# Kernel optimization log

Measured on AMD Instinct MI355X. Metric: run time of the kernel, lower is better.

The kernel has to match this reference:

```python
import jax, jax.numpy as jnp
import numpy as np

B, NCAP, LV, LT, C = 64, 64, 197, 32, 512
NSP = LV - 1          # 196 spatial patches
NUM_KEEP = 98         # ceil(196 * sparse_ratio=0.5)
KEEPED = 49           # int(196 * aggr_ratio=0.5 * sparse_ratio=0.5)
HID = 102             # int(512 * dim_ratio=0.2)
LN_EPS = 1e-5


def _normalize(x):
    # torch F.normalize: x / max(||x||, 1e-12)
    return x / jnp.maximum(jnp.linalg.norm(x, axis=-1, keepdims=True), 1e-12)


def setup_inputs() -> dict:
    key = jax.random.key(0)
    ks = jax.random.split(key, 8)
    def rn(k, shape, s=0.02):
        return jax.random.normal(k, shape, jnp.float32) * s
    return {
        "img_embs": jax.random.normal(ks[0], (B, LV, C), jnp.float32),
        "cap_embs": jax.random.normal(ks[1], (NCAP, LT, C), jnp.float32),
        "cap_lens": jnp.full((NCAP,), LT, jnp.int32),
        "ln_gamma": jnp.ones((C,), jnp.float32),
        "ln_beta": jnp.zeros((C,), jnp.float32),
        "w1": rn(ks[2], (C, HID)), "b1": jnp.zeros((HID,), jnp.float32),
        "w2": rn(ks[3], (HID, KEEPED)), "b2": jnp.zeros((KEEPED,), jnp.float32),
        "aggr_scale": jnp.ones((1, 1, 1), jnp.float32),
        "wi2t": rn(ks[4], (C, C)), "bi2t": jnp.zeros((C,), jnp.float32),
        "wt2i": rn(ks[5], (C, C)), "bt2i": jnp.zeros((C,), jnp.float32),
        "temp": jnp.ones((1, 1, 1), jnp.float32),
    }


def _forward(img_embs, cap_embs, ln_gamma, ln_beta, w1, b1, w2, b2,
             aggr_scale, wi2t, bi2t, wt2i, bt2i, temp):
    img_norm = _normalize(img_embs)
    img_cls = img_embs[:, 0:1]              # [B,1,C]  has_cls_token branch
    img_sp = img_embs[:, 1:]                # [B,196,C]
    img_sp_norm = img_norm[:, 1:]
    # use_cls_as_glob_embd: global = normalized CLS (no grad)
    glo = jax.lax.stop_gradient(img_norm[:, 0:1])
    attn_x = jax.lax.stop_gradient(jnp.sum(glo * img_sp_norm, -1))  # [B,196]
    cap_norm = _normalize(cap_embs)
    bidx = jnp.arange(B)[:, None]

    def ln(x):
        m = x.mean(-1, keepdims=True)
        v = jnp.var(x, axis=-1, keepdims=True)
        return (x - m) / jnp.sqrt(v + LN_EPS) * ln_gamma + ln_beta

    def per_caption(cap_i, cap_i_norm):
        # cap_i, cap_i_norm: [LT, C]
        cap_glo = jax.lax.stop_gradient(_normalize(cap_i[0:1]))           # [1,C]
        attn_y = jax.lax.stop_gradient(jnp.sum(cap_glo[None] * img_sp_norm, -1))  # [B,196]
        # --- TokenSparse ---
        score = attn_x + attn_y
        order = jnp.argsort(-score, axis=1)                              # descending
        keep, nonkeep = order[:, :NUM_KEEP], order[:, NUM_KEEP:]
        sel = img_sp[bidx, keep]                                          # [B,98,C]
        non = img_sp[bidx, nonkeep]                                       # [B,98,C]
        non_score = jnp.take_along_axis(score, nonkeep, 1)
        extra = jnp.sum(non * jax.nn.softmax(non_score, axis=1)[..., None],
                        axis=1, keepdims=True)                            # [B,1,C]
        # --- TokenAggregation ---
        h = jax.nn.gelu(ln(sel) @ w1 + b1, approximate=False)             # [B,98,HID]
        w = jnp.swapaxes(h @ w2 + b2, 1, 2) * aggr_scale                  # [B,49,98]
        aggr = jax.nn.softmax(w, axis=2) @ sel                            # [B,49,C]
        # [cls, aggr, extra] -> [B,51,C], then normalize
        sel_tok = _normalize(jnp.concatenate([img_cls, aggr, extra], 1))
        Ls = sel_tok.shape[1]
        # --- 'attn' similarity ---
        cap_exp = jnp.broadcast_to(cap_i_norm[None], (B, LT, C))
        st = jnp.swapaxes(sel_tok, 1, 2)                                  # [B,C,51]
        c2i = jax.nn.leaky_relu(cap_exp @ st, negative_slope=0.1)         # [B,LT,51]
        a_i2t = jax.nn.softmax((cap_exp @ wi2t + bi2t) @ st / temp, axis=1)
        a_t2i = jax.nn.softmax((cap_exp @ wt2i + bt2i) @ st / temp, axis=2)
        return jnp.sum(a_i2t * c2i / Ls + a_t2i * c2i / LT, axis=(1, 2))  # [B]

    sims = jax.vmap(per_caption)(cap_embs, cap_norm)                      # [NCAP,B]
    return sims.T                                                         # [B,NCAP]


def reference(img_embs, cap_embs, cap_lens, ln_gamma, ln_beta, w1, b1, w2, b2,
              aggr_scale, wi2t, bi2t, wt2i, bt2i, temp):
    # cap_lens are all LT (static shapes); eval-mode output: similarity matrix.
    return _forward(img_embs, cap_embs, ln_gamma, ln_beta, w1, b1, w2, b2,
                    aggr_scale, wi2t, bi2t, wt2i, bt2i, temp)
```

## Files before the change

kernel.cpp:

```cpp
#include <hip/hip_runtime.h>
#include <math.h>

#define B     64
#define NCAP  64
#define LV    197
#define LT    32
#define C     512
#define NSP   196
#define NKEEP 98
#define HID   102
#define KEEPED 49

#define OFF_ATTNX   12608
#define OFF_WSMAT   25152
#define OFF_WT      639808
#define OFF_GLOT    1688384
#define OFF_ATTNYT  1721152
#define OFF_IMGT    14164800
#define OFF_QBB     17834816
#define OFF_QCAP    19407680
#define OFF_W1TF    19931968
#define OFF_W2TF    19960640

typedef unsigned int u32;
typedef unsigned short u16;
typedef __bf16 bf16x8 __attribute__((ext_vector_type(8)));
typedef float f32x4 __attribute__((ext_vector_type(4)));
typedef unsigned int uint4v __attribute__((ext_vector_type(4)));

__device__ __forceinline__ u16 f2bf(float f) {
    u32 u = __builtin_bit_cast(u32, f);
    return (u16)((u + 0x7FFFu + ((u >> 16) & 1u)) >> 16);
}
__device__ __forceinline__ bf16x8 ld_bf8(const u16* p) {
    uint4v v = *reinterpret_cast<const uint4v*>(p);
    return __builtin_bit_cast(bf16x8, v);
}

__device__ __forceinline__ float gelu_exact(float x) {
    return 0.5f * x * (1.f + erff(x * 0.70710678118654752f));
}

__global__ __launch_bounds__(256) void k_pre(const float* __restrict__ img,
                                             const float* __restrict__ cap,
                                             const float* __restrict__ wi2t,
                                             const float* __restrict__ wt2i,
                                             const float* __restrict__ w1,
                                             const float* __restrict__ w2,
                                             u16* __restrict__ imgTf,
                                             float* __restrict__ gloT,
                                             u16* __restrict__ Qbbf,
                                             u16* __restrict__ Qcap,
                                             u16* __restrict__ wT,
                                             u16* __restrict__ w1Tf,
                                             u16* __restrict__ w2Tf) {
    int idx = blockIdx.x, t = threadIdx.x;
    __shared__ __align__(16) u16 shb[64 * 224];

    if (idx < 512) {
        int b = idx >> 3, cg = idx & 7;
        for (int f = t; f < 64 * 27; f += 256) shb[(f / 27) * 224 + 197 + (f % 27)] = 0;
        int cc = t & 63;
        for (int sb = t >> 6; sb < 197; sb += 4) {
            float v = img[((size_t)b * LV + sb) * C + cg * 64 + cc];
            shb[cc * 224 + sb] = f2bf(v);
        }
        __syncthreads();
        const u32* Tu = (const u32*)shb;
        u32* outp = (u32*)imgTf + (size_t)b * 7 * 32 * 256;
        for (int f = t; f < 7 * 4 * 256; f += 256) {
            int ks = f >> 10, rem = f & 1023;
            int ctl = rem >> 8, g = rem & 255;
            int lane_o = g >> 2, j2 = g & 3;
            int quad_o = lane_o >> 4, l15_o = lane_o & 15;
            int ccl = ctl * 16 + l15_o;
            int s = ks * 32 + quad_o * 8 + 2 * j2;
            u32 v = Tu[ccl * 112 + (s >> 1)];
            outp[(size_t)(ks * 32 + cg * 4 + ctl) * 256 + g] = v;
        }
    } else if (idx < 1024) {
        int e = idx - 512, i = e >> 3, tg = e & 7;
        int lane = t & 63, wv = t >> 6;
        int tt = tg * 4 + wv;
        const float* row = cap + ((size_t)i * LT + tt) * C;
        float v[8]; float ss = 0.f;
#pragma unroll
        for (int q = 0; q < 8; ++q) { v[q] = row[lane + 64 * q]; ss += v[q] * v[q]; }
        for (int o = 32; o > 0; o >>= 1) ss += __shfl_down(ss, o);
        ss = __shfl(ss, 0);
        float inv = 1.f / fmaxf(sqrtf(ss), 1e-12f);
        u16* qrow = Qcap + ((size_t)i * 32 + tt) * C;
        int mi = tt >> 4, l15f = tt & 15;
        u16* qfb = Qbbf + (size_t)(i * 6 + mi) * 16 * 512;
#pragma unroll
        for (int q = 0; q < 8; ++q) {
            float n = v[q] * inv;
            u16 nb = f2bf(n);
            int c = lane + 64 * q;
            qrow[c] = nb;
            int ks = c >> 5, quadf = (c >> 3) & 3, jf = c & 7;
            qfb[(size_t)ks * 512 + (quadf * 16 + l15f) * 8 + jf] = nb;
            if (tt == 0) gloT[(c >> 2) * (NCAP * 4) + i * 4 + (c & 3)] = n;
        }
    } else if (idx < 1152) {
        int e = idx - 1024;
        int mat = e >> 6, ty = e & 63, jg = ty >> 3, cg = ty & 7;
        const float* W = mat ? wt2i : wi2t;
        u16 (*tile)[65] = (u16(*)[65])shb;
        for (int f = t; f < 4096; f += 256) {
            int cc2 = f >> 6, jj = f & 63;
            tile[jj][cc2] = f2bf(W[(size_t)(cg * 64 + cc2) * 512 + jg * 64 + jj]);
        }
        __syncthreads();
        for (int f = t; f < 4096; f += 256) {
            int jj = f >> 6, cc2 = f & 63;
            wT[((size_t)mat * 512 + jg * 64 + jj) * 512 + cg * 64 + cc2] = tile[jj][cc2];
        }
    } else if (idx < 1159) {
        int nt = idx - 1152;
        u32* outp = (u32*)w1Tf + (size_t)nt * 16 * 256;
        for (int f = t; f < 16 * 256; f += 256) {
            int ks = f >> 8, g = f & 255;
            int lane_o = g >> 2, j2 = g & 3;
            int l15o = lane_o & 15, quado = lane_o >> 4;
            int kk = ks * 32 + quado * 8 + 2 * j2;
            int n = nt * 16 + l15o;
            u32 lo = 0, hi = 0;
            if (n < HID) {
                lo = f2bf(w1[(size_t)kk * HID + n]);
                hi = f2bf(w1[(size_t)(kk + 1) * HID + n]);
            }
            outp[ks * 256 + g] = lo | (hi << 16);
        }
    } else {
        u32* outp = (u32*)w2Tf;
        for (int f = t; f < 16 * 256; f += 256) {
            int tile = f >> 8, g = f & 255;
            int nt2 = tile >> 2, ks2 = tile & 3;
            int lane_o = g >> 2, j2 = g & 3;
            int l15o = lane_o & 15, quado = lane_o >> 4;
            int kk0 = ks2 * 32 + quado * 8 + 2 * j2;
            int n = nt2 * 16 + l15o;
            u32 lo = 0, hi = 0;
            if (n < KEEPED) {
                if (kk0 < HID)     lo = f2bf(w2[(size_t)kk0 * KEEPED + n]);
                if (kk0 + 1 < HID) hi = f2bf(w2[(size_t)(kk0 + 1) * KEEPED + n]);
            }
            outp[tile * 256 + g] = lo | (hi << 16);
        }
    }
}

__global__ __launch_bounds__(512) void k_mid(const float* __restrict__ img,
                                             const u16* __restrict__ wT,
                                             const float* __restrict__ bi2t,
                                             const float* __restrict__ bt2i,
                                             const u16* __restrict__ Qcap,
                                             u16* __restrict__ Qbbf,
                                             const u16* __restrict__ w1Tf,
                                             const u16* __restrict__ w2Tf,
                                             const float* __restrict__ gamw,
                                             const float* __restrict__ betw,
                                             const float* __restrict__ b1,
                                             const float* __restrict__ b2,
                                             const float* __restrict__ scale_p,
                                             float* __restrict__ attn_x,
                                             float* __restrict__ WsM) {
    int idx = blockIdx.x, t = threadIdx.x;
    __shared__ __align__(16) u16 shu[16 * 520 + 16 * 136];

    if (idx < 256) {
        int i = idx & 63, p = idx >> 6;
        int lane = t & 63, wu = t >> 6;
        int l15 = lane & 15, quad = lane >> 4;
        int mat = wu >> 2;
        int miq = (wu >> 1) & 1;
        int nh  = wu & 1;
        int ni0 = p * 8 + nh * 4;
        const u16* Arow = Qcap + ((size_t)i * 32 + miq * 16 + l15) * 512;
        const u16* Wm   = wT + (size_t)mat * 512 * 512;
        f32x4 acc[4];
#pragma unroll
        for (int n = 0; n < 4; ++n) acc[n] = (f32x4){0.f, 0.f, 0.f, 0.f};
        bf16x8 A = ld_bf8(Arow + quad * 8);
        bf16x8 Bf[4];
#pragma unroll
        for (int n = 0; n < 4; ++n)
            Bf[n] = ld_bf8(Wm + (size_t)((ni0 + n) * 16 + l15) * 512 + quad * 8);
        for (int ks = 0; ks < 16; ++ks) {
            bf16x8 An; bf16x8 Bn[4];
            if (ks < 15) {
                An = ld_bf8(Arow + (ks + 1) * 32 + quad * 8);
#pragma unroll
                for (int n = 0; n < 4; ++n)
                    Bn[n] = ld_bf8(Wm + (size_t)((ni0 + n) * 16 + l15) * 512 + (ks + 1) * 32 + quad * 8);
            }
#pragma unroll
            for (int n = 0; n < 4; ++n)
                acc[n] = __builtin_amdgcn_mfma_f32_16x16x32_bf16(A, Bf[n], acc[n], 0, 0, 0);
            A = An;
#pragma unroll
            for (int n = 0; n < 4; ++n) Bf[n] = Bn[n];
        }
        const float* bias = mat ? bt2i : bi2t;
#pragma unroll
        for (int n = 0; n < 4; ++n) {
            int j = (ni0 + n) * 16 + l15;
            float bj = bias[j];
            int ksf = j >> 5, quadf = (j >> 3) & 3, jf = j & 7;
#pragma unroll
            for (int r = 0; r < 4; ++r) {
                int q = 32 + mat * 32 + miq * 16 + quad * 4 + r;
                int mi = q >> 4, l15f = q & 15;
                Qbbf[(size_t)((i * 6 + mi) * 16 + ksf) * 512 + (quadf * 16 + l15f) * 8 + jf]
                    = f2bf(acc[n][r] + bj);
            }
        }
    } else {
        int e = idx - 256;
        int b = e / 13, sg = e - b * 13;
        int s0 = sg * 16;
        u16* LNb = shu;
        u16* Hb  = shu + 16 * 520;
        int lane = t & 63, wu = t >> 6;
        int l15 = lane & 15, quad = lane >> 4;

        {
            int rr0 = 2 * wu, rr1 = 2 * wu + 1;
            int sA = s0 + rr0, sB = s0 + rr1;
            int sAc = sA < NSP ? sA : NSP - 1;
            int sBc = sB < NSP ? sB : NSP - 1;
            const float* rowA = img + ((size_t)b * LV + 1 + sAc) * C;
            const float* rowB = img + ((size_t)b * LV + 1 + sBc) * C;
            const float* cls  = img + (size_t)b * LV * C;
            float v0[8], v1[8];
            float sm0 = 0, ss0 = 0, dd0 = 0, sm1 = 0, ss1 = 0, dd1 = 0, sc = 0;
#pragma unroll
            for (int q = 0; q < 8; ++q) {
                int c = lane + 64 * q;
                float cv = cls[c];
                v0[q] = rowA[c]; v1[q] = rowB[c];
                sm0 += v0[q]; ss0 += v0[q] * v0[q]; dd0 += v0[q] * cv;
                sm1 += v1[q]; ss1 += v1[q] * v1[q]; dd1 += v1[q] * cv;
                sc  += cv * cv;
            }
            for (int o = 32; o > 0; o >>= 1) {
                sm0 += __shfl_down(sm0, o); ss0 += __shfl_down(ss0, o); dd0 += __shfl_down(dd0, o);
                sm1 += __shfl_down(sm1, o); ss1 += __shfl_down(ss1, o); dd1 += __shfl_down(dd1, o);
                sc  += __shfl_down(sc, o);
            }
            sm0 = __shfl(sm0, 0); ss0 = __shfl(ss0, 0);
            sm1 = __shfl(sm1, 0); ss1 = __shfl(ss1, 0);
            float mean0 = sm0 * (1.f / C);
            float rstd0 = 1.f / sqrtf(ss0 * (1.f / C) - mean0 * mean0 + 1e-5f);
            float mean1 = sm1 * (1.f / C);
            float rstd1 = 1.f / sqrtf(ss1 * (1.f / C) - mean1 * mean1 + 1e-5f);
            if (lane == 0) {
                float inv0 = 1.f / fmaxf(sqrtf(sc), 1e-12f);
                if (sA < NSP) attn_x[b * NSP + sA] = dd0 * inv0 * (1.f / fmaxf(sqrtf(ss0), 1e-12f));
                if (sB < NSP) attn_x[b * NSP + sB] = dd1 * inv0 * (1.f / fmaxf(sqrtf(ss1), 1e-12f));
            }
#pragma unroll
            for (int q = 0; q < 8; ++q) {
                int c = lane + 64 * q;
                float g = gamw[c], be = betw[c];
                LNb[rr0 * 520 + c] = f2bf((v0[q] - mean0) * rstd0 * g + be);
                LNb[rr1 * 520 + c] = f2bf((v1[q] - mean1) * rstd1 * g + be);
            }
        }
        __syncthreads();
        if (wu < 7) {
            const u16* W1b = w1Tf + (size_t)wu * 16 * 512;
            f32x4 h4 = (f32x4){0.f, 0.f, 0.f, 0.f};
            for (int ks = 0; ks < 16; ++ks) {
                bf16x8 A = ld_bf8(LNb + l15 * 520 + ks * 32 + quad * 8);
                bf16x8 Bv = ld_bf8(W1b + ks * 512 + lane * 8);
                h4 = __builtin_amdgcn_mfma_f32_16x16x32_bf16(A, Bv, h4, 0, 0, 0);
            }
            int col = wu * 16 + l15;
            if (col < HID) {
                float bb = b1[col];
#pragma unroll
                for (int r = 0; r < 4; ++r)
                    Hb[(quad * 4 + r) * 136 + col] = f2bf(gelu_exact(h4[r] + bb));
            } else {
#pragma unroll
                for (int r = 0; r < 4; ++r) Hb[(quad * 4 + r) * 136 + col] = 0;
            }
        } else {
            for (int f = lane; f < 16 * 24; f += 64) {
                int row = f / 24, cc = 112 + f % 24;
                Hb[row * 136 + cc] = 0;
            }
        }
        __syncthreads();
        if (wu < 4) {
            const u16* W2b = w2Tf + (size_t)wu * 4 * 512;
            f32x4 a2 = (f32x4){0.f, 0.f, 0.f, 0.f};
            for (int ks2 = 0; ks2 < 4; ++ks2) {
                bf16x8 A2 = ld_bf8(Hb + l15 * 136 + ks2 * 32 + quad * 8);
                bf16x8 B2 = ld_bf8(W2b + ks2 * 512 + lane * 8);
                a2 = __builtin_amdgcn_mfma_f32_16x16x32_bf16(A2, B2, a2, 0, 0, 0);
            }
            int k = wu * 16 + l15;
            if (k < KEEPED) {
                float scale = scale_p[0], bk = b2[k];
#pragma unroll
                for (int r = 0; r < 4; ++r) {
                    int row = quad * 4 + r;
                    if (s0 + row < NSP)
                        WsM[((size_t)b * NSP + s0 + row) * 49 + k] = expf((a2[r] + bk) * scale);
                }
            }
        }
    }
}

__global__ __launch_bounds__(512) void k_midb(const float* __restrict__ img,
                                              const float* __restrict__ gloT,
                                              float* __restrict__ attn_yT) {
    int e = blockIdx.x, t = threadIdx.x;
    int b = e / 25;
    int s0 = (e - b * 25) * 8;
    int R = NSP - s0; if (R > 8) R = 8;
    __shared__ __align__(16) float xr[8][C];
    __shared__ float rnorm[8];

    for (int f = t; f < R * C; f += 512) {
        int rr = f >> 9, c = f & 511;
        xr[rr][c] = img[((size_t)b * LV + 1 + s0 + rr) * C + c];
    }
    __syncthreads();
    {
        int row = t >> 6, l = t & 63;
        if (row < R) {
            float ss = 0.f;
            for (int c = l; c < C; c += 64) { float v = xr[row][c]; ss += v * v; }
            for (int o = 32; o > 0; o >>= 1) ss += __shfl_down(ss, o);
            if (l == 0) rnorm[row] = 1.f / fmaxf(sqrtf(ss), 1e-12f);
        }
    }
    __syncthreads();
    for (int f = t; f < R * C; f += 512) {
        int rr = f >> 9, c = f & 511;
        xr[rr][c] *= rnorm[rr];
    }
    __syncthreads();
    int i = t & 63, w = t >> 6;
    if (w < R) {
        float a0 = 0.f;
        const float4* g4 = (const float4*)gloT;
        const float4* x4 = (const float4*)xr[w];
        for (int c4 = 0; c4 < C / 4; ++c4) {
            float4 g = g4[c4 * NCAP + i];
            float4 x0 = x4[c4];
            a0 += x0.x * g.x + x0.y * g.y + x0.z * g.z + x0.w * g.w;
        }
        attn_yT[((size_t)b * NCAP + i) * NSP + s0 + w] = a0;
    }
}

__global__ __launch_bounds__(512, 4) void k_main(const float* __restrict__ attn_x,
                                                 const float* __restrict__ attn_yT,
                                                 const float* __restrict__ WsM,
                                                 const u16* __restrict__ imgTf,
                                                 const u16* __restrict__ Qbbf,
                                                 const float* __restrict__ temp_p,
                                                 float* __restrict__ out) {
    int lin = blockIdx.x + NCAP * blockIdx.y;
    int b = (lin & 7) * 8 + ((lin >> 3) & 7);
    int i = lin >> 6;
    int t = threadIdx.x;
    int lane = t & 63, wu = t >> 6;
    int l15 = lane & 15, quad = lane >> 4;

    __shared__ __align__(16) u16 TnBuf[51 * 520];
    __shared__ float invn[64];
    __shared__ float redw[8];

    u16*   Pf   = TnBuf;
    float* ULDS = (float*)TnBuf;
    float* scoreS = (float*)(TnBuf + 24000);
    short* rnkH   = (short*)(TnBuf + 24392);
    int*   keepL  = (int*)  (TnBuf + 24784);
    int*   nonL   = (int*)  (TnBuf + 24980);
    float* snon   = (float*)(TnBuf + 25176);
    float* rowsq  = (float*)(TnBuf + 25372);

    {
        uint4v* Pfv = (uint4v*)Pf;
        for (int f = t; f < 51 * 232 / 8; f += 512) Pfv[f] = (uint4v){0, 0, 0, 0};
    }
    if (t < NSP)
        scoreS[t] = attn_x[b * NSP + t] + attn_yT[((size_t)b * NCAP + i) * NSP + t];
    __syncthreads();
    if (t < 2 * NSP) {
        int half = (t >= NSP) ? 1 : 0;
        int s = t - half * NSP;
        float sv = scoreS[s];
        const float2* sc2 = (const float2*)scoreS;
        int base = half ? 49 : 0;
        int r = 0;
        for (int u2 = base; u2 < base + 49; ++u2) {
            float2 o = sc2[u2];
            int u = 2 * u2;
            r += (o.x > sv) || (o.x == sv && u < s);
            r += (o.y > sv) || (o.y == sv && (u + 1) < s);
        }
        rnkH[half * NSP + s] = (short)r;
    }
    __syncthreads();
    if (t < NSP) {
        int r = rnkH[t] + rnkH[NSP + t];
        if (r < NKEEP) keepL[r] = t;
        else { nonL[r - NKEEP] = t; snon[r - NKEEP] = scoreS[t]; }
    }
    __syncthreads();
    if (t == 0) Pf[0] = 0x3F80;
    {
        int j = t / KEEPED, k = t - (t / KEEPED) * KEEPED;
        while (j < NKEEP) {
            int s = keepL[j];
            Pf[(1 + k) * 232 + 1 + s] = f2bf(WsM[((size_t)b * NSP + s) * KEEPED + k]);
            j += 10; k += 22;
            if (k >= KEEPED) { k -= KEEPED; ++j; }
        }
    }
    if (t < NKEEP) Pf[50 * 232 + 1 + nonL[t]] = f2bf(expf(snon[t]));
    __syncthreads();

    const u16* imgTb = imgTf + (size_t)b * 7 * 32 * 512;
    f32x4 acc[4][4];
#pragma unroll
    for (int mi = 0; mi < 4; ++mi)
#pragma unroll
        for (int nj = 0; nj < 4; ++nj) acc[mi][nj] = (f32x4){0.f, 0.f, 0.f, 0.f};

    {
        bf16x8 Bc[4], Bn[4];
#pragma unroll
        for (int nj = 0; nj < 4; ++nj)
            Bc[nj] = ld_bf8(imgTb + (size_t)(wu * 4 + nj) * 512 + lane * 8);
        for (int ks = 0; ks < 7; ++ks) {
            if (ks < 6) {
#pragma unroll
                for (int nj = 0; nj < 4; ++nj)
                    Bn[nj] = ld_bf8(imgTb + (size_t)((ks + 1) * 32 + wu * 4 + nj) * 512 + lane * 8);
            }
            bf16x8 Afr[4];
#pragma unroll
            for (int mi = 0; mi < 4; ++mi)
                Afr[mi] = ld_bf8(Pf + (mi * 16 + l15) * 232 + ks * 32 + quad * 8);
#pragma unroll
            for (int nj = 0; nj < 4; ++nj)
#pragma unroll
                for (int mi = 0; mi < 4; ++mi)
                    acc[mi][nj] = __builtin_amdgcn_mfma_f32_16x16x32_bf16(Afr[mi], Bc[nj], acc[mi][nj], 0, 0, 0);
#pragma unroll
            for (int nj = 0; nj < 4; ++nj) Bc[nj] = Bn[nj];
        }
    }

#pragma unroll
    for (int mi = 0; mi < 4; ++mi)
#pragma unroll
        for (int r = 0; r < 4; ++r) {
            float s = acc[mi][0][r] * acc[mi][0][r] + acc[mi][1][r] * acc[mi][1][r]
                    + acc[mi][2][r] * acc[mi][2][r] + acc[mi][3][r] * acc[mi][3][r];
            s += __shfl_down(s, 8); s += __shfl_down(s, 4);
            s += __shfl_down(s, 2); s += __shfl_down(s, 1);
            if (l15 == 0) rowsq[wu * 64 + mi * 16 + quad * 4 + r] = s;
        }
    __syncthreads();
    if (t < 64) {
        float s = 0.f;
#pragma unroll
        for (int w2 = 0; w2 < 8; ++w2) s += rowsq[w2 * 64 + t];
        invn[t] = 1.f / fmaxf(sqrtf(s), 1e-12f);
    }
    __syncthreads();

#pragma unroll
    for (int mi = 0; mi < 4; ++mi)
#pragma unroll
        for (int r = 0; r < 4; ++r) {
            int row = mi * 16 + quad * 4 + r;
            if (row < 51) {
                float iv = invn[row];
#pragma unroll
                for (int nj = 0; nj < 4; ++nj)
                    TnBuf[row * 520 + (wu * 4 + nj) * 16 + l15] = f2bf(acc[mi][nj][r] * iv);
            }
        }
    __syncthreads();

    const u16* Qbf = Qbbf + (size_t)i * 6 * 16 * 512;
    f32x4 ua[3];
#pragma unroll
    for (int e = 0; e < 3; ++e) ua[e] = (f32x4){0.f, 0.f, 0.f, 0.f};

    if (wu < 6) {
        int mi = wu;
        const u16* Ar = Qbf + (size_t)mi * 16 * 512 + lane * 8;
        bf16x8 Af = ld_bf8(Ar);
        for (int ks = 0; ks < 16; ++ks) {
            bf16x8 An;
            if (ks < 15) An = ld_bf8(Ar + (ks + 1) * 512);
#pragma unroll
            for (int e = 0; e < 3; ++e) {
                bf16x8 Bf = ld_bf8(TnBuf + (e * 16 + l15) * 520 + ks * 32 + quad * 8);
                ua[e] = __builtin_amdgcn_mfma_f32_16x16x32_bf16(Af, Bf, ua[e], 0, 0, 0);
            }
            Af = An;
        }
    } else {
        int w2 = wu - 6;
        int rowB = 48 + l15; if (rowB > 50) rowB = 50;
        const u16* Ar0 = Qbf + (size_t)(3 * w2 + 0) * 16 * 512 + lane * 8;
        const u16* Ar1 = Qbf + (size_t)(3 * w2 + 1) * 16 * 512 + lane * 8;
        const u16* Ar2 = Qbf + (size_t)(3 * w2 + 2) * 16 * 512 + lane * 8;
        bf16x8 Af0 = ld_bf8(Ar0);
        bf16x8 Af1 = ld_bf8(Ar1);
        bf16x8 Af2 = ld_bf8(Ar2);
        for (int ks = 0; ks < 16; ++ks) {
            bf16x8 An0, An1, An2;
            if (ks < 15) {
                An0 = ld_bf8(Ar0 + (ks + 1) * 512);
                An1 = ld_bf8(Ar1 + (ks + 1) * 512);
                An2 = ld_bf8(Ar2 + (ks + 1) * 512);
            }
            bf16x8 Bf = ld_bf8(TnBuf + rowB * 520 + ks * 32 + quad * 8);
            ua[0] = __builtin_amdgcn_mfma_f32_16x16x32_bf16(Af0, Bf, ua[0], 0, 0, 0);
            ua[1] = __builtin_amdgcn_mfma_f32_16x16x32_bf16(Af1, Bf, ua[1], 0, 0, 0);
            ua[2] = __builtin_amdgcn_mfma_f32_16x16x32_bf16(Af2, Bf, ua[2], 0, 0, 0);
            Af0 = An0; Af1 = An1; Af2 = An2;
        }
    }
    __syncthreads();

    if (wu < 6) {
#pragma unroll
        for (int e = 0; e < 3; ++e) {
            int l = e * 16 + l15;
            int q0 = wu * 16 + quad * 4;
#pragma unroll
            for (int r = 0; r < 4; ++r) ULDS[(q0 + r) * 52 + l] = ua[e][r];
        }
    } else {
        int l = 48 + l15;
        if (l < 51) {
            int w2 = wu - 6;
#pragma unroll
            for (int e = 0; e < 3; ++e) {
                int q0 = (3 * w2 + e) * 16 + quad * 4;
#pragma unroll
                for (int r = 0; r < 4; ++r) ULDS[(q0 + r) * 52 + l] = ua[e][r];
            }
        }
    }
    __syncthreads();

    float invT = 1.f / temp_p[0];
    if (t < 408) {
        int l = t >> 3, sub = t & 7;
        float vbuf[4]; float mm = -1e30f;
#pragma unroll
        for (int q = 0; q < 4; ++q) {
            float v = ULDS[(32 + sub + 8 * q) * 52 + l] * invT;
            vbuf[q] = v;
            mm = fmaxf(mm, v);
        }
#pragma unroll
        for (int o = 1; o < 8; o <<= 1) mm = fmaxf(mm, __shfl_xor(mm, o, 8));
        float e[4]; float z = 0.f;
#pragma unroll
        for (int q = 0; q < 4; ++q) { e[q] = expf(vbuf[q] - mm); z += e[q]; }
#pragma unroll
        for (int o = 1; o < 8; o <<= 1) z += __shfl_xor(z, o, 8);
        float iz = 1.f / z;
#pragma unroll
        for (int q = 0; q < 4; ++q) ULDS[(32 + sub + 8 * q) * 52 + l] = e[q] * iz;
    }
    if (t < 256) {
        int u = t >> 3, sub = t & 7;
        float vbuf[7]; int cnt = 0; float mm = -1e30f;
        for (int l = sub; l < 51; l += 8) {
            float v = ULDS[(64 + u) * 52 + l] * invT;
            vbuf[cnt++] = v;
            mm = fmaxf(mm, v);
        }
#pragma unroll
        for (int o = 1; o < 8; o <<= 1) mm = fmaxf(mm, __shfl_xor(mm, o, 8));
        float e[7]; float z = 0.f;
        for (int q = 0; q < cnt; ++q) { e[q] = expf(vbuf[q] - mm); z += e[q]; }
#pragma unroll
        for (int o = 1; o < 8; o <<= 1) z += __shfl_xor(z, o, 8);
        float iz = 1.f / z;
        { int q = 0;
          for (int l = sub; l < 51; l += 8) { ULDS[(64 + u) * 52 + l] = e[q] * iz; ++q; } }
    }
    __syncthreads();

    float part = 0.f;
    {
        int u = t / 51, l = t - (t / 51) * 51;
        while (u < LT) {
            float u0 = ULDS[u * 52 + l];
            float c2 = (u0 > 0.f) ? u0 : 0.1f * u0;
            float av = ULDS[(32 + u) * 52 + l];
            float bv = ULDS[(64 + u) * 52 + l];
            part += c2 * (av * (1.f / 51.f) + bv * (1.f / 32.f));
            u += 10; l += 2;
            if (l >= 51) { l -= 51; ++u; }
        }
    }
    for (int o = 32; o > 0; o >>= 1) part += __shfl_down(part, o);
    if (lane == 0) redw[wu] = part;
    __syncthreads();
    if (t == 0) {
        float s = 0.f;
#pragma unroll
        for (int w2 = 0; w2 < 8; ++w2) s += redw[w2];
        out[b * NCAP + i] = s;
    }
}

extern "C" void kernel_launch(void* const* d_in, const int* in_sizes, int n_in,
                              void* d_out, int out_size, void* d_ws, size_t ws_size,
                              hipStream_t stream) {
    const float* img        = (const float*)d_in[0];
    const float* cap        = (const float*)d_in[1];
    const float* gamw       = (const float*)d_in[3];
    const float* betw       = (const float*)d_in[4];
    const float* w1         = (const float*)d_in[5];
    const float* b1         = (const float*)d_in[6];
    const float* w2         = (const float*)d_in[7];
    const float* b2         = (const float*)d_in[8];
    const float* aggr_scale = (const float*)d_in[9];
    const float* wi2t       = (const float*)d_in[10];
    const float* bi2t       = (const float*)d_in[11];
    const float* wt2i       = (const float*)d_in[12];
    const float* bt2i       = (const float*)d_in[13];
    const float* temp       = (const float*)d_in[14];
    float* out = (float*)d_out;

    float* ws      = (float*)d_ws;
    float* attn_x  = ws + OFF_ATTNX;
    float* WsM     = ws + OFF_WSMAT;
    u16*   wT      = (u16*)(ws + OFF_WT);
    float* gloT    = ws + OFF_GLOT;
    float* attn_yT = ws + OFF_ATTNYT;
    u16*   imgTf   = (u16*)(ws + OFF_IMGT);
    u16*   Qbbf    = (u16*)(ws + OFF_QBB);
    u16*   Qcap    = (u16*)(ws + OFF_QCAP);
    u16*   w1Tf    = (u16*)(ws + OFF_W1TF);
    u16*   w2Tf    = (u16*)(ws + OFF_W2TF);

    k_pre<<<dim3(1160), dim3(256), 0, stream>>>(img, cap, wi2t, wt2i, w1, w2,
                                                imgTf, gloT, Qbbf, Qcap, wT, w1Tf, w2Tf);
    k_mid<<<dim3(1088), dim3(512), 0, stream>>>(img, wT, bi2t, bt2i, Qcap, Qbbf,
                                                w1Tf, w2Tf, gamw, betw, b1, b2, aggr_scale,
                                                attn_x, WsM);
    k_midb<<<dim3(1600), dim3(512), 0, stream>>>(img, gloT, attn_yT);
    k_main<<<dim3(NCAP, B), dim3(512), 0, stream>>>(attn_x, attn_yT, WsM, imgTf, Qbbf, temp, out);
}
```

Before: 353.3 us.

## Split top-k ranking into separate kernel and store aggregation weights in bf16

Moves the per-(image,caption) score ranking and keep/non-keep partitioning out of k_main into a new k_rank kernel that writes index lists and bf16 exp scores to workspace. k_main now only gathers these lists, reads a bf16 WsM buffer written directly by k_mid, and issues its first imgT B-fragment loads before the LDS setup so they overlap. The aim is to shorten the serial rank phase inside the MFMA-heavy main kernel and halve WsM traffic. The cost is an extra launch plus a global round trip for the index lists.

```diff
diff --git a/kernel.cpp b/kernel.cpp
--- a/kernel.cpp
+++ b/kernel.cpp
@@ -21,6 +21,9 @@
 #define OFF_QCAP    19407680
 #define OFF_W1TF    19931968
 #define OFF_W2TF    19960640
+#define OFF_KEEPG   19964736
+#define OFF_NONSG   20165440
+#define OFF_NONEG   20366144
 
 typedef unsigned int u32;
 typedef unsigned short u16;
@@ -165,7 +168,7 @@
                                              const float* __restrict__ b2,
                                              const float* __restrict__ scale_p,
                                              float* __restrict__ attn_x,
-                                             float* __restrict__ WsM) {
+                                             u16* __restrict__ WsM16) {
     int idx = blockIdx.x, t = threadIdx.x;
     __shared__ __align__(16) u16 shu[16 * 520 + 16 * 136];
 
@@ -309,7 +312,7 @@
                 for (int r = 0; r < 4; ++r) {
                     int row = quad * 4 + r;
                     if (s0 + row < NSP)
-                        WsM[((size_t)b * NSP + s0 + row) * 49 + k] = expf((a2[r] + bk) * scale);
+                        WsM16[((size_t)b * NSP + s0 + row) * 49 + k] = f2bf(expf((a2[r] + bk) * scale));
                 }
             }
         }
@@ -360,43 +363,23 @@
     }
 }
 
-__global__ __launch_bounds__(512, 4) void k_main(const float* __restrict__ attn_x,
-                                                 const float* __restrict__ attn_yT,
-                                                 const float* __restrict__ WsM,
-                                                 const u16* __restrict__ imgTf,
-                                                 const u16* __restrict__ Qbbf,
-                                                 const float* __restrict__ temp_p,
-                                                 float* __restrict__ out) {
-    int lin = blockIdx.x + NCAP * blockIdx.y;
-    int b = (lin & 7) * 8 + ((lin >> 3) & 7);
-    int i = lin >> 6;
+__global__ __launch_bounds__(256) void k_rank(const float* __restrict__ attn_x,
+                                              const float* __restrict__ attn_yT,
+                                              u16* __restrict__ keepG,
+                                              u16* __restrict__ nonSG,
+                                              u16* __restrict__ nonEG) {
+    int pair = blockIdx.x;
+    int b = pair >> 6, i = pair & 63;
     int t = threadIdx.x;
-    int lane = t & 63, wu = t >> 6;
-    int l15 = lane & 15, quad = lane >> 4;
-
-    __shared__ __align__(16) u16 TnBuf[51 * 520];
-    __shared__ float invn[64];
-    __shared__ float redw[8];
-
-    u16*   Pf   = TnBuf;
-    float* ULDS = (float*)TnBuf;
-    float* scoreS = (float*)(TnBuf + 24000);
-    short* rnkH   = (short*)(TnBuf + 24392);
-    int*   keepL  = (int*)  (TnBuf + 24784);
-    int*   nonL   = (int*)  (TnBuf + 24980);
-    float* snon   = (float*)(TnBuf + 25176);
-    float* rowsq  = (float*)(TnBuf + 25372);
-
-    {
-        uint4v* Pfv = (uint4v*)Pf;
-        for (int f = t; f < 51 * 232 / 8; f += 512) Pfv[f] = (uint4v){0, 0, 0, 0};
-    }
+    __shared__ float scoreS[NSP];
+    __shared__ short rnkH[2 * NSP];
+
     if (t < NSP)
         scoreS[t] = attn_x[b * NSP + t] + attn_yT[((size_t)b * NCAP + i) * NSP + t];
     __syncthreads();
-    if (t < 2 * NSP) {
-        int half = (t >= NSP) ? 1 : 0;
-        int s = t - half * NSP;
+    for (int task = t; task < 2 * NSP; task += 256) {
+        int half = (task >= NSP) ? 1 : 0;
+        int s = task - half * NSP;
         float sv = scoreS[s];
         const float2* sc2 = (const float2*)scoreS;
         int base = half ? 49 : 0;
@@ -412,53 +395,88 @@
     __syncthreads();
     if (t < NSP) {
         int r = rnkH[t] + rnkH[NSP + t];
-        if (r < NKEEP) keepL[r] = t;
-        else { nonL[r - NKEEP] = t; snon[r - NKEEP] = scoreS[t]; }
-    }
+        if (r < NKEEP) keepG[(size_t)pair * NKEEP + r] = (u16)t;
+        else {
+            int p = r - NKEEP;
+            nonSG[(size_t)pair * NKEEP + p] = (u16)t;
+            nonEG[(size_t)pair * NKEEP + p] = f2bf(expf(scoreS[t]));
+        }
+    }
+}
+
+__global__ __launch_bounds__(512, 4) void k_main(const u16* __restrict__ WsM16,
+                                                 const u16* __restrict__ imgTf,
+                                                 const u16* __restrict__ Qbbf,
+                                                 const u16* __restrict__ keepG,
+                                                 const u16* __restrict__ nonSG,
+                                                 const u16* __restrict__ nonEG,
+                                                 const float* __restrict__ temp_p,
+                                                 float* __restrict__ out) {
+    int lin = blockIdx.x + NCAP * blockIdx.y;
+    int b = (lin & 7) * 8 + ((lin >> 3) & 7);
+    int i = lin >> 6;
+    int pair = b * NCAP + i;
+    int t = threadIdx.x;
+    int lane = t & 63, wu = t >> 6;
+    int l15 = lane & 15, quad = lane >> 4;
+
+    __shared__ __align__(16) u16 TnBuf[51 * 520];
+    __shared__ float invn[64];
+    __shared__ float redw[8];
+
+    u16*   Pf   = TnBuf;
+    float* ULDS = (float*)TnBuf;
+    u16*   kL    = (u16*)  (TnBuf + 24000);
+    float* rowsq = (float*)(TnBuf + 25372);
+
+    const u16* imgTb = imgTf + (size_t)b * 7 * 32 * 512;
+    bf16x8 Bc[4], Bn[4];
+#pragma unroll
+    for (int nj = 0; nj < 4; ++nj)
+        Bc[nj] = ld_bf8(imgTb + (size_t)(wu * 4 + nj) * 512 + lane * 8);
+
+    {
+        uint4v* Pfv = (uint4v*)Pf;
+        for (int f = t; f < 51 * 232 / 8; f += 512) Pfv[f] = (uint4v){0, 0, 0, 0};
+    }
+    if (t < NKEEP) kL[t] = keepG[(size_t)pair * NKEEP + t];
     __syncthreads();
     if (t == 0) Pf[0] = 0x3F80;
+    if (t < NKEEP) Pf[50 * 232 + 1 + nonSG[(size_t)pair * NKEEP + t]] = nonEG[(size_t)pair * NKEEP + t];
     {
         int j = t / KEEPED, k = t - (t / KEEPED) * KEEPED;
         while (j < NKEEP) {
-            int s = keepL[j];
-            Pf[(1 + k) * 232 + 1 + s] = f2bf(WsM[((size_t)b * NSP + s) * KEEPED + k]);
+            int s = kL[j];
+            Pf[(1 + k) * 232 + 1 + s] = WsM16[((size_t)b * NSP + s) * 49 + k];
             j += 10; k += 22;
             if (k >= KEEPED) { k -= KEEPED; ++j; }
         }
     }
-    if (t < NKEEP) Pf[50 * 232 + 1 + nonL[t]] = f2bf(expf(snon[t]));
-    __syncthreads();
-
-    const u16* imgTb = imgTf + (size_t)b * 7 * 32 * 512;
+    __syncthreads();
+
     f32x4 acc[4][4];
 #pragma unroll
     for (int mi = 0; mi < 4; ++mi)
 #pragma unroll
         for (int nj = 0; nj < 4; ++nj) acc[mi][nj] = (f32x4){0.f, 0.f, 0.f, 0.f};
 
-    {
-        bf16x8 Bc[4], Bn[4];
+    for (int ks = 0; ks < 7; ++ks) {
+        if (ks < 6) {
+#pragma unroll
+            for (int nj = 0; nj < 4; ++nj)
+                Bn[nj] = ld_bf8(imgTb + (size_t)((ks + 1) * 32 + wu * 4 + nj) * 512 + lane * 8);
+        }
+        bf16x8 Afr[4];
+#pragma unroll
+        for (int mi = 0; mi < 4; ++mi)
+            Afr[mi] = ld_bf8(Pf + (mi * 16 + l15) * 232 + ks * 32 + quad * 8);
 #pragma unroll
         for (int nj = 0; nj < 4; ++nj)
-            Bc[nj] = ld_bf8(imgTb + (size_t)(wu * 4 + nj) * 512 + lane * 8);
-        for (int ks = 0; ks < 7; ++ks) {
-            if (ks < 6) {
-#pragma unroll
-                for (int nj = 0; nj < 4; ++nj)
-                    Bn[nj] = ld_bf8(imgTb + (size_t)((ks + 1) * 32 + wu * 4 + nj) * 512 + lane * 8);
-            }
-            bf16x8 Afr[4];
 #pragma unroll
             for (int mi = 0; mi < 4; ++mi)
-                Afr[mi] = ld_bf8(Pf + (mi * 16 + l15) * 232 + ks * 32 + quad * 8);
-#pragma unroll
-            for (int nj = 0; nj < 4; ++nj)
-#pragma unroll
-                for (int mi = 0; mi < 4; ++mi)
-                    acc[mi][nj] = __builtin_amdgcn_mfma_f32_16x16x32_bf16(Afr[mi], Bc[nj], acc[mi][nj], 0, 0, 0);
-#pragma unroll
-            for (int nj = 0; nj < 4; ++nj) Bc[nj] = Bn[nj];
-        }
+                acc[mi][nj] = __builtin_amdgcn_mfma_f32_16x16x32_bf16(Afr[mi], Bc[nj], acc[mi][nj], 0, 0, 0);
+#pragma unroll
+        for (int nj = 0; nj < 4; ++nj) Bc[nj] = Bn[nj];
     }
 
 #pragma unroll
@@ -646,7 +664,7 @@
 
     float* ws      = (float*)d_ws;
     float* attn_x  = ws + OFF_ATTNX;
-    float* WsM     = ws + OFF_WSMAT;
+    u16*   WsM16   = (u16*)(ws + OFF_WSMAT);
     u16*   wT      = (u16*)(ws + OFF_WT);
     float* gloT    = ws + OFF_GLOT;
     float* attn_yT = ws + OFF_ATTNYT;
@@ -655,12 +673,16 @@
     u16*   Qcap    = (u16*)(ws + OFF_QCAP);
     u16*   w1Tf    = (u16*)(ws + OFF_W1TF);
     u16*   w2Tf    = (u16*)(ws + OFF_W2TF);
+    u16*   keepG   = (u16*)(ws + OFF_KEEPG);
+    u16*   nonSG   = (u16*)(ws + OFF_NONSG);
+    u16*   nonEG   = (u16*)(ws + OFF_NONEG);
 
     k_pre<<<dim3(1160), dim3(256), 0, stream>>>(img, cap, wi2t, wt2i, w1, w2,
                                                 imgTf, gloT, Qbbf, Qcap, wT, w1Tf, w2Tf);
     k_mid<<<dim3(1088), dim3(512), 0, stream>>>(img, wT, bi2t, bt2i, Qcap, Qbbf,
                                                 w1Tf, w2Tf, gamw, betw, b1, b2, aggr_scale,
-                                                attn_x, WsM);
+                                                attn_x, WsM16);
     k_midb<<<dim3(1600), dim3(512), 0, stream>>>(img, gloT, attn_yT);
-    k_main<<<dim3(NCAP, B), dim3(512), 0, stream>>>(attn_x, attn_yT, WsM, imgTf, Qbbf, temp, out);
-}
+    k_rank<<<dim3(4096), dim3(256), 0, stream>>>(attn_x, attn_yT, keepG, nonSG, nonEG);
+    k_main<<<dim3(NCAP, B), dim3(512), 0, stream>>>(WsM16, imgTf, Qbbf, keepG, nonSG, nonEG, temp, out);
+}
```

Result: slower. 363.2 us (+2.8%).
